# Optimization experiments

Measured on AMD Instinct MI355X. Metric: run time of the kernel, lower is better.

## Reference

```python
import jax, jax.numpy as jnp
import numpy as np

N = 100000      # nodes
E = 1600000     # edges (before self-loops)
F_IN = 128      # input feature dim (lazy in GATConv, chosen here)
H1, H2 = 64, 2  # out channels of conv1 / conv2 (heads=1)
NEG_SLOPE = 0.2
BN_EPS = 1e-5


def _glorot(key, shape):
    lim = np.sqrt(6.0 / (shape[0] + shape[-1]))
    return jax.random.uniform(key, shape, jnp.float32, -lim, lim)


def setup_inputs() -> dict:
    key = jax.random.key(0)
    ks = jax.random.split(key, 12)
    x = jax.random.normal(ks[0], (N, F_IN), jnp.float32)
    edge_index = jax.random.randint(ks[1], (2, E), 0, N, dtype=jnp.int64)
    return {
        "x": x,
        "edge_index": edge_index,
        "W1_src": _glorot(ks[2], (F_IN, H1)),
        "W1_dst": _glorot(ks[3], (F_IN, H1)),
        "a1_src": _glorot(ks[4], (H1,)),
        "a1_dst": _glorot(ks[5], (H1,)),
        "b1": jnp.zeros((H1,), jnp.float32),
        "gamma": jnp.ones((H1,), jnp.float32),
        "beta": jnp.zeros((H1,), jnp.float32),
        "W2_src": _glorot(ks[6], (H1, H2)),
        "W2_dst": _glorot(ks[7], (H1, H2)),
        "a2_src": _glorot(ks[8], (H2,)),
        "a2_dst": _glorot(ks[9], (H2,)),
        "b2": jnp.zeros((H2,), jnp.float32),
    }


def gat_layer(x, src, dst, W_src, W_dst, a_src, a_dst, b):
    n = x.shape[0]
    hs = x @ W_src                     # [N, C] source-side projection
    hd = x @ W_dst                     # [N, C] target-side projection
    alpha_s = hs @ a_src               # [N]
    alpha_d = hd @ a_dst               # [N]
    e = jax.nn.leaky_relu(alpha_s[src] + alpha_d[dst], NEG_SLOPE)  # [E']
    # segment softmax over edges grouped by target node (every node has a self-loop)
    m = jax.ops.segment_max(e, dst, num_segments=n)
    p = jnp.exp(e - m[dst])
    s = jax.ops.segment_sum(p, dst, num_segments=n)
    alpha = p / (s[dst] + 1e-16)
    out = jax.ops.segment_sum(hs[src] * alpha[:, None], dst, num_segments=n)
    return out + b


def reference(x, edge_index, W1_src, W1_dst, a1_src, a1_dst, b1,
              gamma, beta, W2_src, W2_dst, a2_src, a2_dst, b2):
    loops = jnp.arange(N, dtype=edge_index.dtype)
    ei = jnp.concatenate([edge_index, jnp.stack([loops, loops])], axis=1)
    src, dst = ei[0], ei[1]
    h = gat_layer(x, src, dst, W1_src, W1_dst, a1_src, a1_dst, b1)
    # BatchNorm1d (training mode: batch stats, biased variance)
    mu = h.mean(axis=0)
    var = ((h - mu) ** 2).mean(axis=0)
    h = gamma * (h - mu) * jax.lax.rsqrt(var + BN_EPS) + beta
    h = jax.nn.relu(h)
    return gat_layer(h, src, dst, W2_src, W2_dst, a2_src, a2_dst, b2)
```

## Files before the change

kernel.cpp:

```cpp
#include <hip/hip_runtime.h>
#include <hip/hip_fp16.h>
#include <math.h>

#define NODES 100000
#define NEDGE 1600000
#define ETOT  (NEDGE + NODES)
#define FIN   128
#define C1    64
#define NEG   0.2f
#define BNEPS 1e-5f
#define BNBLK 512
#define PSCALE 0.00390625f

#define BK     128
#define NBUCK  ((NODES + BK - 1) / BK)
#define PCAP   2816
#define PTILE  4096
#define GB1    ((NODES + 63) / 64)
#define PB     ((NEDGE + PTILE - 1) / PTILE)

typedef __attribute__((ext_vector_type(8))) short bf16x8;
typedef __attribute__((ext_vector_type(4))) float f32x4;

static __device__ __forceinline__ short f2bf(float f) {
    unsigned u = __builtin_bit_cast(unsigned, f);
    unsigned r = (u + 0x7FFFu + ((u >> 16) & 1u)) >> 16;
    return (short)r;
}


__global__ __launch_bounds__(256) void k_prep(const float* __restrict__ W1s,
                                              const float* __restrict__ W1d, const float* __restrict__ a1d,
                                              const float* __restrict__ W2d, const float* __restrict__ a2d,
                                              float* wad1, float* wad2, unsigned short* __restrict__ wfrag,
                                              int* __restrict__ bcur) {
    int t = threadIdx.x;
    int b = blockIdx.x;
    if (b == 33) {
        for (int i = t; i < NBUCK; i += 256) bcur[i] = 0;
    } else if (b == 32) {
        if (t < FIN) {
            float acc = 0.f;
            for (int c = 0; c < C1; c++) acc = fmaf(W1d[t * C1 + c], a1d[c], acc);
            wad1[t] = acc;
        }
        if (t < C1) {
            wad2[t] = fmaf(W2d[t * 2], a2d[0], W2d[t * 2 + 1] * a2d[1]);
        }
    } else {
        int idx = b * 256 + t;
        int j  = idx & 7;
        int ln = (idx >> 3) & 63;
        int it = (idx >> 9) & 3;
        int ct = idx >> 11;
        int k  = it * 32 + (ln >> 4) * 8 + j;
        int ch = ct * 16 + (ln & 15);
        wfrag[idx] = (unsigned short)f2bf(W1s[k * C1 + ch]);
    }
}


__device__ __forceinline__ void gemm1_body(int blk, const float* __restrict__ x,
                                           const unsigned short* __restrict__ wfrag,
                                           const float* __restrict__ wad, const float* __restrict__ a_src,
                                           __half* __restrict__ hsh, float* __restrict__ as_out,
                                           float* __restrict__ ad_out) {
    int t = threadIdx.x;
    int lane = t & 63;
    int wv = t >> 6;
    int n0 = blk * 64 + wv * 16;
    int li = lane & 15, g = lane >> 4;

    int row = n0 + li;
    bool rv = row < NODES;
    const float* xr = x + (size_t)row * FIN + g * 8;

    f32x4 acc0 = {0.f,0.f,0.f,0.f}, acc1 = {0.f,0.f,0.f,0.f};
    f32x4 acc2 = {0.f,0.f,0.f,0.f}, acc3 = {0.f,0.f,0.f,0.f};
    bf16x8 af[4];
    float adp = 0.f;

    #pragma unroll
    for (int it = 0; it < 4; it++) {
        float xv[8];
        if (rv) {
            float4 lo = *reinterpret_cast<const float4*>(xr + it * 32);
            float4 hi = *reinterpret_cast<const float4*>(xr + it * 32 + 4);
            xv[0]=lo.x; xv[1]=lo.y; xv[2]=lo.z; xv[3]=lo.w;
            xv[4]=hi.x; xv[5]=hi.y; xv[6]=hi.z; xv[7]=hi.w;
        } else {
            #pragma unroll
            for (int j = 0; j < 8; j++) xv[j] = 0.f;
        }
        const float* wr = wad + g * 8 + it * 32;
        float4 wlo = *reinterpret_cast<const float4*>(wr);
        float4 whi = *reinterpret_cast<const float4*>(wr + 4);
        adp = fmaf(xv[0], wlo.x, adp); adp = fmaf(xv[1], wlo.y, adp);
        adp = fmaf(xv[2], wlo.z, adp); adp = fmaf(xv[3], wlo.w, adp);
        adp = fmaf(xv[4], whi.x, adp); adp = fmaf(xv[5], whi.y, adp);
        adp = fmaf(xv[6], whi.z, adp); adp = fmaf(xv[7], whi.w, adp);
        bf16x8 a;
        #pragma unroll
        for (int j = 0; j < 8; j++) a[j] = f2bf(xv[j]);
        af[it] = a;
    }

    const bf16x8* wfv = reinterpret_cast<const bf16x8*>(wfrag);
    #pragma unroll
    for (int it = 0; it < 4; it++) {
        acc0 = __builtin_amdgcn_mfma_f32_16x16x32_bf16(af[it], wfv[(0*4+it)*64 + lane], acc0, 0, 0, 0);
        acc1 = __builtin_amdgcn_mfma_f32_16x16x32_bf16(af[it], wfv[(1*4+it)*64 + lane], acc1, 0, 0, 0);
        acc2 = __builtin_amdgcn_mfma_f32_16x16x32_bf16(af[it], wfv[(2*4+it)*64 + lane], acc2, 0, 0, 0);
        acc3 = __builtin_amdgcn_mfma_f32_16x16x32_bf16(af[it], wfv[(3*4+it)*64 + lane], acc3, 0, 0, 0);
    }

    adp += __shfl_xor(adp, 16);
    adp += __shfl_xor(adp, 32);
    if (lane < 16 && rv) ad_out[row] = adp;

    float a0 = a_src[0 * 16 + li], a1 = a_src[1 * 16 + li];
    float a2 = a_src[2 * 16 + li], a3 = a_src[3 * 16 + li];
    float asp0 = acc0[0]*a0 + acc1[0]*a1 + acc2[0]*a2 + acc3[0]*a3;
    float asp1 = acc0[1]*a0 + acc1[1]*a1 + acc2[1]*a2 + acc3[1]*a3;
    float asp2 = acc0[2]*a0 + acc1[2]*a1 + acc2[2]*a2 + acc3[2]*a3;
    float asp3 = acc0[3]*a0 + acc1[3]*a1 + acc2[3]*a2 + acc3[3]*a3;
    #pragma unroll
    for (int o = 1; o <= 8; o <<= 1) {
        asp0 += __shfl_xor(asp0, o);
        asp1 += __shfl_xor(asp1, o);
        asp2 += __shfl_xor(asp2, o);
        asp3 += __shfl_xor(asp3, o);
    }
    if ((lane & 12) == 0) {
        int r = lane & 3;
        int n = n0 + 4 * g + r;
        if (n < NODES) {
            float av = (r == 0) ? asp0 : (r == 1) ? asp1 : (r == 2) ? asp2 : asp3;
            as_out[n] = av;
        }
    }

    #pragma unroll
    for (int r = 0; r < 4; r++) {
        int n = n0 + 4 * g + r;
        if (n < NODES) {
            __half* hb = hsh + (size_t)n * C1 + li;
            hb[ 0] = __float2half(acc0[r]);
            hb[16] = __float2half(acc1[r]);
            hb[32] = __float2half(acc2[r]);
            hb[48] = __float2half(acc3[r]);
        }
    }
}

__global__ __launch_bounds__(256) void k_fused1(const float* __restrict__ x,
                                                const unsigned short* __restrict__ wfrag,
                                                const float* __restrict__ wad, const float* __restrict__ a_src,
                                                __half* __restrict__ hsh, float* __restrict__ as_out,
                                                float* __restrict__ ad_out,
                                                const int* __restrict__ ei, int* bcur,
                                                unsigned* __restrict__ tmp) {
    __shared__ int hist[NBUCK], hbase[NBUCK];
    if (blockIdx.x < GB1) {
        gemm1_body(blockIdx.x, x, wfrag, wad, a_src, hsh, as_out, ad_out);
        return;
    }
    int t = threadIdx.x;
    for (int i = t; i < NBUCK; i += 256) hist[i] = 0;
    __syncthreads();
    const int* srcs = ei;
    const int* dsts = ei + NEDGE;
    int e_base = (blockIdx.x - GB1) * PTILE;
    unsigned pack[16];
    int bkt[16], slot[16];
    #pragma unroll
    for (int i = 0; i < 16; i++) {
        int e = e_base + i * 256 + t;
        bool valid = e < NEDGE;
        int s = valid ? srcs[e] : 0;
        int d = valid ? dsts[e] : 0;
        if ((unsigned)d >= NODES || (unsigned)s >= NODES) valid = false;
        bkt[i] = valid ? (d >> 7) : -1;
        pack[i] = (unsigned)s | ((unsigned)(d & (BK - 1)) << 17);
        slot[i] = valid ? atomicAdd(&hist[bkt[i]], 1) : -1;
    }
    __syncthreads();
    for (int i = t; i < NBUCK; i += 256)
        hbase[i] = hist[i] ? atomicAdd(&bcur[i], hist[i]) : 0;
    __syncthreads();
    #pragma unroll
    for (int i = 0; i < 16; i++) {
        if (slot[i] >= 0) {
            int pos = hbase[bkt[i]] + slot[i];
            if (pos < PCAP) tmp[(size_t)bkt[i] * PCAP + pos] = pack[i];
        }
    }
}

__global__ __launch_bounds__(256) void k_build(const unsigned* __restrict__ tmp, const int* __restrict__ bcur,
                                               const float* __restrict__ as1, const float* __restrict__ ad1,
                                               int* __restrict__ offs, int* __restrict__ csr,
                                               uint2* __restrict__ pe) {
    __shared__ int cnt[BK];
    __shared__ int ps_[BK];
    __shared__ int red[256];
    __shared__ int stage[PCAP + BK];
    int t = threadIdx.x;
    int b = blockIdx.x;
    int ecnt = bcur[b]; if (ecnt > PCAP) ecnt = PCAP;

    int part = 0;
    for (int i = t; i < b; i += 256) part += bcur[i];
    red[t] = part;
    __syncthreads();
    for (int o = 128; o; o >>= 1) {
        if (t < o) red[t] += red[t + o];
        __syncthreads();
    }
    int csrbase = red[0] + BK * b;
    const unsigned* ebuf = tmp + (size_t)b * PCAP;

    if (t < BK) cnt[t] = 0;
    __syncthreads();
    for (int e = t; e < ecnt; e += 256) {
        int dl = (ebuf[e] >> 17) & (BK - 1);
        atomicAdd(&cnt[dl], 1);
    }
    __syncthreads();
    int gn = b * BK + t;
    int own = 0;
    if (t < BK) {
        own = cnt[t] + ((gn < NODES) ? 1 : 0);
        ps_[t] = own;
    }
    __syncthreads();
    for (int o = 1; o < BK; o <<= 1) {
        int add = (t < BK && t >= o) ? ps_[t - o] : 0;
        __syncthreads();
        if (t < BK) ps_[t] += add;
        __syncthreads();
    }
    int total = ps_[BK - 1];
    if (t < BK && gn < NODES) {
        int excl = ps_[t] - own;
        stage[excl] = gn | (t << 17);
        cnt[t] = excl + 1;
        offs[gn] = csrbase + excl;
    }
    if (b == NBUCK - 1 && t == 0) offs[NODES] = ETOT;
    if (b == NBUCK - 1 && t < 16) pe[ETOT + t] = make_uint2(0u, 0u);
    __syncthreads();
    for (int e = t; e < ecnt; e += 256) {
        unsigned p = ebuf[e];
        int dl = (p >> 17) & (BK - 1);
        int slot = atomicAdd(&cnt[dl], 1);
        stage[slot] = (int)p;
    }
    __syncthreads();
    for (int j = t; j < total; j += 256) {
        int v = stage[j];
        int s = v & 0x1FFFF;
        int d = b * BK + (int)(((unsigned)v) >> 17);
        csr[csrbase + j] = s;
        float e = as1[s] + ad1[d];
        e = e > 0.f ? e : NEG * e;
        float p = __expf(fminf(e, 60.f));
        pe[csrbase + j] = make_uint2((unsigned)s, __float_as_uint(p));
    }
}


__global__ __launch_bounds__(256) void k_agg1(const int* __restrict__ offs, const uint2* __restrict__ pe,
                                              const __half* __restrict__ hsh, const float* __restrict__ b1,
                                              __half* __restrict__ h1h) {
    int w = threadIdx.x >> 6, lane = threadIdx.x & 63;
    int node = blockIdx.x * 4 + w;
    if (node >= NODES) return;
    int e0 = offs[node], e1 = offs[node + 1];
    int g = lane >> 4, l = lane & 15;
    __half2 acc01 = __floats2half2_rn(0.f, 0.f);
    __half2 acc23 = __floats2half2_rn(0.f, 0.f);
    float ssum = 0.f;
    for (int base = e0; base < e1; base += 16) {
        int ea = base + g, eb = ea + 4, ec = ea + 8, ed = ea + 12;
        uint2 spa = pe[ea];
        uint2 spb = pe[eb];
        uint2 spc = pe[ec];
        uint2 spd = pe[ed];
        float pa = ea < e1 ? __uint_as_float(spa.y) : 0.f;
        float pb = eb < e1 ? __uint_as_float(spb.y) : 0.f;
        float pc = ec < e1 ? __uint_as_float(spc.y) : 0.f;
        float pd = ed < e1 ? __uint_as_float(spd.y) : 0.f;
        uint2 ra = *reinterpret_cast<const uint2*>(hsh + (size_t)spa.x * C1 + l * 4);
        uint2 rb = *reinterpret_cast<const uint2*>(hsh + (size_t)spb.x * C1 + l * 4);
        uint2 rc = *reinterpret_cast<const uint2*>(hsh + (size_t)spc.x * C1 + l * 4);
        uint2 rd = *reinterpret_cast<const uint2*>(hsh + (size_t)spd.x * C1 + l * 4);
        ssum += (pa + pb) + (pc + pd);
        __half2 pha = __float2half2_rn(pa * PSCALE);
        __half2 phb = __float2half2_rn(pb * PSCALE);
        __half2 phc = __float2half2_rn(pc * PSCALE);
        __half2 phd = __float2half2_rn(pd * PSCALE);
        acc01 = __hfma2(pha, *reinterpret_cast<const __half2*>(&ra.x), acc01);
        acc23 = __hfma2(pha, *reinterpret_cast<const __half2*>(&ra.y), acc23);
        acc01 = __hfma2(phb, *reinterpret_cast<const __half2*>(&rb.x), acc01);
        acc23 = __hfma2(phb, *reinterpret_cast<const __half2*>(&rb.y), acc23);
        acc01 = __hfma2(phc, *reinterpret_cast<const __half2*>(&rc.x), acc01);
        acc23 = __hfma2(phc, *reinterpret_cast<const __half2*>(&rc.y), acc23);
        acc01 = __hfma2(phd, *reinterpret_cast<const __half2*>(&rd.x), acc01);
        acc23 = __hfma2(phd, *reinterpret_cast<const __half2*>(&rd.y), acc23);
    }
    ssum += __shfl_xor(ssum, 16); ssum += __shfl_xor(ssum, 32);
    unsigned u01 = *reinterpret_cast<unsigned*>(&acc01);
    unsigned u23 = *reinterpret_cast<unsigned*>(&acc23);
    unsigned v01 = (unsigned)__shfl_xor((int)u01, 16);
    unsigned v23 = (unsigned)__shfl_xor((int)u23, 16);
    acc01 = __hadd2(acc01, *reinterpret_cast<__half2*>(&v01));
    acc23 = __hadd2(acc23, *reinterpret_cast<__half2*>(&v23));
    u01 = *reinterpret_cast<unsigned*>(&acc01);
    u23 = *reinterpret_cast<unsigned*>(&acc23);
    v01 = (unsigned)__shfl_xor((int)u01, 32);
    v23 = (unsigned)__shfl_xor((int)u23, 32);
    acc01 = __hadd2(acc01, *reinterpret_cast<__half2*>(&v01));
    acc23 = __hadd2(acc23, *reinterpret_cast<__half2*>(&v23));
    if (g == 0) {
        float inv = 256.0f / (ssum + 1e-16f);
        float2 f01 = __half22float2(acc01);
        float2 f23 = __half22float2(acc23);
        float4 bv = reinterpret_cast<const float4*>(b1)[l];
        __half2 r01 = __floats2half2_rn(fmaf(f01.x, inv, bv.x), fmaf(f01.y, inv, bv.y));
        __half2 r23 = __floats2half2_rn(fmaf(f23.x, inv, bv.z), fmaf(f23.y, inv, bv.w));
        uint2 packed = make_uint2(*reinterpret_cast<unsigned*>(&r01), *reinterpret_cast<unsigned*>(&r23));
        reinterpret_cast<uint2*>(h1h + (size_t)node * C1)[l] = packed;
    }
}


__global__ __launch_bounds__(256) void k_bnstats(const __half* __restrict__ h1h, float* __restrict__ bnpart) {
    __shared__ float red[256][8];
    int t = threadIdx.x;
    const uint2* hv = reinterpret_cast<const uint2*>(h1h);
    const int total = NODES * 16;
    float s0=0.f,s1=0.f,s2=0.f,s3=0.f,q0=0.f,q1=0.f,q2=0.f,q3=0.f;
    for (int i = blockIdx.x * 256 + t; i < total; i += BNBLK * 256) {
        uint2 u = hv[i];
        float2 a = __half22float2(*reinterpret_cast<const __half2*>(&u.x));
        float2 b = __half22float2(*reinterpret_cast<const __half2*>(&u.y));
        s0 += a.x; q0 = fmaf(a.x, a.x, q0);
        s1 += a.y; q1 = fmaf(a.y, a.y, q1);
        s2 += b.x; q2 = fmaf(b.x, b.x, q2);
        s3 += b.y; q3 = fmaf(b.y, b.y, q3);
    }
    red[t][0]=s0; red[t][1]=s1; red[t][2]=s2; red[t][3]=s3;
    red[t][4]=q0; red[t][5]=q1; red[t][6]=q2; red[t][7]=q3;
    __syncthreads();
    if (t < 64) {
        int quad = t >> 2, j = t & 3;
        float ts = 0.f, tq = 0.f;
        #pragma unroll
        for (int k = 0; k < 16; k++) {
            ts += red[k * 16 + quad][j];
            tq += red[k * 16 + quad][j + 4];
        }
        bnpart[(size_t)blockIdx.x * 128 + t]      = ts;
        bnpart[(size_t)blockIdx.x * 128 + 64 + t] = tq;
    }
}


__global__ __launch_bounds__(256) void k_bngemm2(const __half* __restrict__ h1h, const float* __restrict__ bnpart,
                                                 const float* __restrict__ gamma, const float* __restrict__ beta,
                                                 const float* __restrict__ W2s,
                                                 const float* __restrict__ wad2, const float* __restrict__ a2s,
                                                 float* __restrict__ hs2, float* __restrict__ as2,
                                                 float* __restrict__ ad2) {
    __shared__ float sc_s[64], sh_s[64];
    int t = threadIdx.x;
    if (t < 64) {
        float s = 0.f, q = 0.f;
        for (int b = 0; b < BNBLK; b++) {
            s += bnpart[(size_t)b * 128 + t];
            q += bnpart[(size_t)b * 128 + 64 + t];
        }
        float mu = s * (1.0f / NODES);
        float var = q * (1.0f / NODES) - mu * mu;
        if (var < 0.f) var = 0.f;
        float rinv = 1.0f / sqrtf(var + BNEPS);
        float sc = gamma[t] * rinv;
        sc_s[t] = sc;
        sh_s[t] = beta[t] - mu * sc;
    }
    __syncthreads();
    int n = blockIdx.x * 256 + t;
    if (n >= NODES) return;
    const uint2* hr = reinterpret_cast<const uint2*>(h1h + (size_t)n * C1);
    float h0 = 0.f, h1v = 0.f, adv = 0.f;
    #pragma unroll
    for (int c4 = 0; c4 < 16; c4++) {
        uint2 u = hr[c4];
        float2 v01 = __half22float2(*reinterpret_cast<const __half2*>(&u.x));
        float2 v23 = __half22float2(*reinterpret_cast<const __half2*>(&u.y));
        float vv[4] = {v01.x, v01.y, v23.x, v23.y};
        #pragma unroll
        for (int j = 0; j < 4; j++) {
            int c = c4 * 4 + j;
            float y = fmaf(vv[j], sc_s[c], sh_s[c]);
            y = fmaxf(y, 0.f);
            h0 = fmaf(y, W2s[c * 2 + 0], h0);
            h1v = fmaf(y, W2s[c * 2 + 1], h1v);
            adv = fmaf(y, wad2[c], adv);
        }
    }
    hs2[n * 2 + 0] = h0;
    hs2[n * 2 + 1] = h1v;
    as2[n] = fmaf(h0, a2s[0], h1v * a2s[1]);
    ad2[n] = adv;
}


__global__ __launch_bounds__(256) void k_agg2(const int* __restrict__ offs, const int* __restrict__ csr,
                                              const float* __restrict__ as2, const float* __restrict__ ad2,
                                              const float* __restrict__ hs2, const float* __restrict__ b2,
                                              float* __restrict__ out) {
    int sub = threadIdx.x >> 4, l = threadIdx.x & 15;
    int node = blockIdx.x * 16 + sub;
    if (node >= NODES) return;
    int e0 = offs[node], e1 = offs[node + 1];
    float adn = ad2[node];
    float ssum = 0.f, A0 = 0.f, A1 = 0.f;
    const float2* h2 = reinterpret_cast<const float2*>(hs2);
    for (int e = e0 + l; e < e1; e += 16) {
        int s = csr[e];
        float v = as2[s] + adn;
        v = v > 0.f ? v : NEG * v;
        float p = __expf(fminf(v, 60.f));
        ssum += p;
        float2 hv = h2[s];
        A0 = fmaf(p, hv.x, A0);
        A1 = fmaf(p, hv.y, A1);
    }
    #pragma unroll
    for (int o = 1; o < 16; o <<= 1) {
        ssum += __shfl_xor(ssum, o);
        A0   += __shfl_xor(A0, o);
        A1   += __shfl_xor(A1, o);
    }
    if (l == 0) {
        float inv = 1.0f / (ssum + 1e-16f);
        float2 r = make_float2(fmaf(A0, inv, b2[0]), fmaf(A1, inv, b2[1]));
        reinterpret_cast<float2*>(out)[node] = r;
    }
}


static inline size_t align256(size_t x) { return (x + 255) & ~size_t(255); }

extern "C" void kernel_launch(void* const* d_in, const int* in_sizes, int n_in,
                              void* d_out, int out_size, void* d_ws, size_t ws_size,
                              hipStream_t stream) {
    const float* x     = (const float*)d_in[0];
    const int*   ei    = (const int*)d_in[1];
    const float* W1s   = (const float*)d_in[2];
    const float* W1d   = (const float*)d_in[3];
    const float* a1s   = (const float*)d_in[4];
    const float* a1d   = (const float*)d_in[5];
    const float* b1    = (const float*)d_in[6];
    const float* gamma = (const float*)d_in[7];
    const float* beta  = (const float*)d_in[8];
    const float* W2s   = (const float*)d_in[9];
    const float* W2d   = (const float*)d_in[10];
    const float* a2s   = (const float*)d_in[11];
    const float* a2d   = (const float*)d_in[12];
    const float* b2    = (const float*)d_in[13];
    float* out = (float*)d_out;

    char* w = (char*)d_ws;
    size_t off = 0;
    auto alloc = [&](size_t bytes) -> void* {
        void* p = w + off;
        off = align256(off + bytes);
        return p;
    };
    int* offs     = (int*)alloc((size_t)(NODES + 1) * 4);
    int* bcur     = (int*)alloc((size_t)NBUCK * 4);
    int* csr      = (int*)alloc((size_t)ETOT * 4);
    uint2* pe     = (uint2*)alloc((size_t)(ETOT + 16) * 8);
    __half* hs1h  = (__half*)alloc((size_t)NODES * C1 * 2);
    float* as1    = (float*)alloc((size_t)NODES * 4);
    float* ad1    = (float*)alloc((size_t)NODES * 4);
    __half* h1h   = (__half*)alloc((size_t)NODES * C1 * 2);
    float* csrtmp_own = (float*)alloc((size_t)NBUCK * PCAP * 4);
    float* hs2    = (float*)alloc((size_t)NODES * 2 * 4);
    float* as2    = (float*)alloc((size_t)NODES * 4);
    float* ad2    = (float*)alloc((size_t)NODES * 4);
    float* wad1   = (float*)alloc(FIN * 4);
    float* wad2   = (float*)alloc(C1 * 4);
    unsigned short* wfrag = (unsigned short*)alloc(8192 * 2);
    float* bnpart = (float*)alloc((size_t)BNBLK * 128 * 4);
    if (off > ws_size) return;

    unsigned* csr_tmp = (unsigned*)csrtmp_own;

    k_prep<<<34, 256, 0, stream>>>(W1s, W1d, a1d, W2d, a2d, wad1, wad2, wfrag, bcur);
    k_fused1<<<GB1 + PB, 256, 0, stream>>>(x, wfrag, wad1, a1s, hs1h, as1, ad1, ei, bcur, csr_tmp);
    k_build<<<NBUCK, 256, 0, stream>>>(csr_tmp, bcur, as1, ad1, offs, csr, pe);
    k_agg1<<<(NODES + 3) / 4, 256, 0, stream>>>(offs, pe, hs1h, b1, h1h);
    k_bnstats<<<BNBLK, 256, 0, stream>>>(h1h, bnpart);
    k_bngemm2<<<(NODES + 255) / 256, 256, 0, stream>>>(h1h, bnpart, gamma, beta, W2s, wad2, a2s, hs2, as2, ad2);
    k_agg2<<<(NODES + 15) / 16, 256, 0, stream>>>(offs, csr, as2, ad2, hs2, b2, out);
}
```

Baseline: 144.1 us.

## Pack source index and bf16 edge weight into one 32-bit word per edge

The per-edge record becomes a single 32-bit word holding a 17-bit source index and a truncated 15-bit bf16 of the exponentiated score. This replaces the separate int CSR array and the 8-byte uint2 array. agg1 now loads four packed edges per 16-byte vector from an aligned base, masking edges outside the node's range, and agg2 reads source indices from the same packed array. The aim is to cut edge-stream memory traffic and write bandwidth in build, at the cost of reduced precision on the attention weights (sign bit dropped, bf16 mantissa).

```diff
diff --git a/kernel.cpp b/kernel.cpp
--- a/kernel.cpp
+++ b/kernel.cpp
@@ -199,8 +199,7 @@
 
 __global__ __launch_bounds__(256) void k_build(const unsigned* __restrict__ tmp, const int* __restrict__ bcur,
                                                const float* __restrict__ as1, const float* __restrict__ ad1,
-                                               int* __restrict__ offs, int* __restrict__ csr,
-                                               uint2* __restrict__ pe) {
+                                               int* __restrict__ offs, unsigned* __restrict__ pe4) {
     __shared__ int cnt[BK];
     __shared__ int ps_[BK];
     __shared__ int red[256];
@@ -248,7 +247,7 @@
         offs[gn] = csrbase + excl;
     }
     if (b == NBUCK - 1 && t == 0) offs[NODES] = ETOT;
-    if (b == NBUCK - 1 && t < 16) pe[ETOT + t] = make_uint2(0u, 0u);
+    if (b == NBUCK - 1 && t < 32) pe4[ETOT + t] = 0u;
     __syncthreads();
     for (int e = t; e < ecnt; e += 256) {
         unsigned p = ebuf[e];
@@ -261,16 +260,16 @@
         int v = stage[j];
         int s = v & 0x1FFFF;
         int d = b * BK + (int)(((unsigned)v) >> 17);
-        csr[csrbase + j] = s;
         float e = as1[s] + ad1[d];
         e = e > 0.f ? e : NEG * e;
         float p = __expf(fminf(e, 60.f));
-        pe[csrbase + j] = make_uint2((unsigned)s, __float_as_uint(p));
-    }
-}
-
-
-__global__ __launch_bounds__(256) void k_agg1(const int* __restrict__ offs, const uint2* __restrict__ pe,
+        unsigned bf = ((unsigned)(unsigned short)f2bf(p)) & 0x7FFFu;
+        pe4[csrbase + j] = (unsigned)s | (bf << 17);
+    }
+}
+
+
+__global__ __launch_bounds__(256) void k_agg1(const int* __restrict__ offs, const unsigned* __restrict__ pe4,
                                               const __half* __restrict__ hsh, const float* __restrict__ b1,
                                               __half* __restrict__ h1h) {
     int w = threadIdx.x >> 6, lane = threadIdx.x & 63;
@@ -281,33 +280,24 @@
     __half2 acc01 = __floats2half2_rn(0.f, 0.f);
     __half2 acc23 = __floats2half2_rn(0.f, 0.f);
     float ssum = 0.f;
-    for (int base = e0; base < e1; base += 16) {
-        int ea = base + g, eb = ea + 4, ec = ea + 8, ed = ea + 12;
-        uint2 spa = pe[ea];
-        uint2 spb = pe[eb];
-        uint2 spc = pe[ec];
-        uint2 spd = pe[ed];
-        float pa = ea < e1 ? __uint_as_float(spa.y) : 0.f;
-        float pb = eb < e1 ? __uint_as_float(spb.y) : 0.f;
-        float pc = ec < e1 ? __uint_as_float(spc.y) : 0.f;
-        float pd = ed < e1 ? __uint_as_float(spd.y) : 0.f;
-        uint2 ra = *reinterpret_cast<const uint2*>(hsh + (size_t)spa.x * C1 + l * 4);
-        uint2 rb = *reinterpret_cast<const uint2*>(hsh + (size_t)spb.x * C1 + l * 4);
-        uint2 rc = *reinterpret_cast<const uint2*>(hsh + (size_t)spc.x * C1 + l * 4);
-        uint2 rd = *reinterpret_cast<const uint2*>(hsh + (size_t)spd.x * C1 + l * 4);
-        ssum += (pa + pb) + (pc + pd);
-        __half2 pha = __float2half2_rn(pa * PSCALE);
-        __half2 phb = __float2half2_rn(pb * PSCALE);
-        __half2 phc = __float2half2_rn(pc * PSCALE);
-        __half2 phd = __float2half2_rn(pd * PSCALE);
-        acc01 = __hfma2(pha, *reinterpret_cast<const __half2*>(&ra.x), acc01);
-        acc23 = __hfma2(pha, *reinterpret_cast<const __half2*>(&ra.y), acc23);
-        acc01 = __hfma2(phb, *reinterpret_cast<const __half2*>(&rb.x), acc01);
-        acc23 = __hfma2(phb, *reinterpret_cast<const __half2*>(&rb.y), acc23);
-        acc01 = __hfma2(phc, *reinterpret_cast<const __half2*>(&rc.x), acc01);
-        acc23 = __hfma2(phc, *reinterpret_cast<const __half2*>(&rc.y), acc23);
-        acc01 = __hfma2(phd, *reinterpret_cast<const __half2*>(&rd.x), acc01);
-        acc23 = __hfma2(phd, *reinterpret_cast<const __half2*>(&rd.y), acc23);
+    int base0 = e0 & ~15;
+    for (int base = base0; base < e1; base += 16) {
+        int eg = base + 4 * g;
+        uint4 q = *reinterpret_cast<const uint4*>(pe4 + eg);
+        unsigned wv[4] = {q.x, q.y, q.z, q.w};
+        #pragma unroll
+        for (int j = 0; j < 4; j++) {
+            int e = eg + j;
+            bool valid = (e >= e0) && (e < e1);
+            unsigned ww = wv[j];
+            float p = valid ? __uint_as_float((ww >> 17) << 16) : 0.f;
+            int s = valid ? (int)(ww & 0x1FFFFu) : 0;
+            uint2 r = *reinterpret_cast<const uint2*>(hsh + (size_t)s * C1 + l * 4);
+            ssum += p;
+            __half2 ph = __float2half2_rn(p * PSCALE);
+            acc01 = __hfma2(ph, *reinterpret_cast<const __half2*>(&r.x), acc01);
+            acc23 = __hfma2(ph, *reinterpret_cast<const __half2*>(&r.y), acc23);
+        }
     }
     ssum += __shfl_xor(ssum, 16); ssum += __shfl_xor(ssum, 32);
     unsigned u01 = *reinterpret_cast<unsigned*>(&acc01);
@@ -417,7 +407,7 @@
 }
 
 
-__global__ __launch_bounds__(256) void k_agg2(const int* __restrict__ offs, const int* __restrict__ csr,
+__global__ __launch_bounds__(256) void k_agg2(const int* __restrict__ offs, const unsigned* __restrict__ pe4,
                                               const float* __restrict__ as2, const float* __restrict__ ad2,
                                               const float* __restrict__ hs2, const float* __restrict__ b2,
                                               float* __restrict__ out) {
@@ -429,7 +419,7 @@
     float ssum = 0.f, A0 = 0.f, A1 = 0.f;
     const float2* h2 = reinterpret_cast<const float2*>(hs2);
     for (int e = e0 + l; e < e1; e += 16) {
-        int s = csr[e];
+        int s = (int)(pe4[e] & 0x1FFFFu);
         float v = as2[s] + adn;
         v = v > 0.f ? v : NEG * v;
         float p = __expf(fminf(v, 60.f));
@@ -482,8 +472,7 @@
     };
     int* offs     = (int*)alloc((size_t)(NODES + 1) * 4);
     int* bcur     = (int*)alloc((size_t)NBUCK * 4);
-    int* csr      = (int*)alloc((size_t)ETOT * 4);
-    uint2* pe     = (uint2*)alloc((size_t)(ETOT + 16) * 8);
+    unsigned* pe4 = (unsigned*)alloc((size_t)(ETOT + 32) * 4);
     __half* hs1h  = (__half*)alloc((size_t)NODES * C1 * 2);
     float* as1    = (float*)alloc((size_t)NODES * 4);
     float* ad1    = (float*)alloc((size_t)NODES * 4);
@@ -502,9 +491,9 @@
 
     k_prep<<<34, 256, 0, stream>>>(W1s, W1d, a1d, W2d, a2d, wad1, wad2, wfrag, bcur);
     k_fused1<<<GB1 + PB, 256, 0, stream>>>(x, wfrag, wad1, a1s, hs1h, as1, ad1, ei, bcur, csr_tmp);
-    k_build<<<NBUCK, 256, 0, stream>>>(csr_tmp, bcur, as1, ad1, offs, csr, pe);
-    k_agg1<<<(NODES + 3) / 4, 256, 0, stream>>>(offs, pe, hs1h, b1, h1h);
+    k_build<<<NBUCK, 256, 0, stream>>>(csr_tmp, bcur, as1, ad1, offs, pe4);
+    k_agg1<<<(NODES + 3) / 4, 256, 0, stream>>>(offs, pe4, hs1h, b1, h1h);
     k_bnstats<<<BNBLK, 256, 0, stream>>>(h1h, bnpart);
     k_bngemm2<<<(NODES + 255) / 256, 256, 0, stream>>>(h1h, bnpart, gamma, beta, W2s, wad2, a2s, hs2, as2, ad2);
-    k_agg2<<<(NODES + 15) / 16, 256, 0, stream>>>(offs, csr, as2, ad2, hs2, b2, out);
-}
+    k_agg2<<<(NODES + 15) / 16, 256, 0, stream>>>(offs, pe4, as2, ad2, hs2, b2, out);
+}
```

Result: no change. 142.6 us (-1.0%).
